# Optimization experiments

Measured on AMD Instinct MI355X. Metric: run time of the kernel, lower is better.

Reference implementation:

```python
import jax, jax.numpy as jnp
import numpy as np

N = 50000
D_IN = 128
D_OUT = 128
EPS = 1e-5


def setup_inputs() -> dict:
    key = jax.random.key(0)
    ks = jax.random.split(key, 10)
    x = jax.random.normal(ks[0], (N, D_IN), dtype=jnp.float32)
    edge_index = jax.random.randint(ks[1], (2, 800000), 0, N, dtype=jnp.int64)
    s_in = 1.0 / np.sqrt(D_IN)
    s_out = 1.0 / np.sqrt(D_OUT)
    return {
        "x": x,
        "edge_index": edge_index,
        # SAGEConv 1: lin_l (on aggregated neighbors, with bias), lin_r (root, no bias)
        "w1_l": jax.random.uniform(ks[2], (D_OUT, D_IN), jnp.float32, -s_in, s_in),
        "b1_l": jnp.zeros((D_OUT,), jnp.float32),
        "w1_r": jax.random.uniform(ks[3], (D_OUT, D_IN), jnp.float32, -s_in, s_in),
        # SAGEConv 2
        "w2_l": jax.random.uniform(ks[4], (D_OUT, D_OUT), jnp.float32, -s_out, s_out),
        "b2_l": jnp.zeros((D_OUT,), jnp.float32),
        "w2_r": jax.random.uniform(ks[5], (D_OUT, D_OUT), jnp.float32, -s_out, s_out),
        # BatchNorm affine params
        "bn_gamma": jnp.ones((D_OUT,), jnp.float32),
        "bn_beta": jnp.zeros((D_OUT,), jnp.float32),
    }


def _sage_conv(x, src, dst, w_l, b_l, w_r):
    # mean aggregation of source-node features into target nodes
    msg = x[src]                                              # [E, D]
    agg = jax.ops.segment_sum(msg, dst, num_segments=N)       # [N, D]
    cnt = jax.ops.segment_sum(jnp.ones((src.shape[0],), x.dtype), dst, num_segments=N)
    mean = agg / jnp.maximum(cnt, 1.0)[:, None]
    return mean @ w_l.T + b_l + x @ w_r.T


def _batch_norm(x, gamma, beta):
    mu = jnp.mean(x, axis=0)
    var = jnp.mean(jnp.square(x - mu), axis=0)  # biased, as in torch BN training
    return (x - mu) * jax.lax.rsqrt(var + EPS) * gamma + beta


def reference(x, edge_index, w1_l, b1_l, w1_r, w2_l, b2_l, w2_r, bn_gamma, bn_beta):
    src, dst = edge_index[0], edge_index[1]
    h = _sage_conv(x, src, dst, w1_l, b1_l, w1_r)
    h = _batch_norm(h, bn_gamma, bn_beta)
    h = jax.nn.relu(h)
    out = _sage_conv(h, src, dst, w2_l, b2_l, w2_r)
    return out
```

## Files before the change

kernel.cpp:

```cpp
#include <hip/hip_runtime.h>

#define D 128
#define EPS 1e-5f
#define FB_EPB 8

typedef unsigned int uint;
typedef __attribute__((ext_vector_type(4))) float f32x4;
typedef __attribute__((ext_vector_type(8))) short s16x8;

__device__ __forceinline__ uint pack_bf16(float a, float b)
{
    uint ua = __float_as_uint(a);
    uint ub = __float_as_uint(b);
    ua += 0x7FFFu + ((ua >> 16) & 1u);
    ub += 0x7FFFu + ((ub >> 16) & 1u);
    return (ua >> 16) | (ub & 0xFFFF0000u);
}
__device__ __forceinline__ float bf_lo(uint v) { return __uint_as_float(v << 16); }
__device__ __forceinline__ float bf_hi(uint v) { return __uint_as_float(v & 0xFFFF0000u); }

__global__ void prep_kernel(const float* __restrict__ x, uint* __restrict__ xb, int ncvt,
                            const float* __restrict__ w1l, const float* __restrict__ w1r,
                            const float* __restrict__ w2l, const float* __restrict__ w2r,
                            uint* __restrict__ wb1, uint* __restrict__ wb2)
{
    int idx = blockIdx.x * 256 + threadIdx.x;
    if (idx < ncvt) {
        float4 v = ((const float4*)x)[idx];
        uint2 o;
        o.x = pack_bf16(v.x, v.y);
        o.y = pack_bf16(v.z, v.w);
        ((uint2*)xb)[idx] = o;
    } else if (idx < ncvt + 8192) {
        int r = idx - ncvt;
        int layer = r >> 12;
        int rem = r & 4095;
        int lane = rem & 63;
        int knt = rem >> 6;
        int kstep = knt >> 3, nt = knt & 7;
        int nn = nt * 16 + (lane & 15);
        int kbase = kstep * 32 + (lane >> 4) * 8;
        const float* wl = layer ? w2l : w1l;
        const float* wr = layer ? w2r : w1r;
        uint* wb = layer ? wb2 : wb1;
        float v[8];
#pragma unroll
        for (int j = 0; j < 8; j++) {
            int k = kbase + j;
            v[j] = (k < D) ? wl[nn * D + k] : wr[nn * D + (k - D)];
        }
        uint4 o;
        o.x = pack_bf16(v[0], v[1]);
        o.y = pack_bf16(v[2], v[3]);
        o.z = pack_bf16(v[4], v[5]);
        o.w = pack_bf16(v[6], v[7]);
        ((uint4*)wb)[(kstep * 8 + nt) * 64 + lane] = o;
    } else if (idx < ncvt + 8192 + 32) {
        ((uint2*)xb)[ncvt + (idx - ncvt - 8192)] = make_uint2(0, 0);
    }
}

__global__ __launch_bounds__(512) void bcount_kernel(const int* __restrict__ dst,
                                                     int* __restrict__ bcnt,
                                                     int E, int nblk, int nbuck)
{
    __shared__ int cnt[128];
    int t = threadIdx.x;
    if (t < 128) cnt[t] = 0;
    __syncthreads();
    int e0 = blockIdx.x * (512 * FB_EPB);
#pragma unroll
    for (int k = 0; k < FB_EPB; k++) {
        int e = e0 + k * 512 + t;
        if (e < E) atomicAdd(&cnt[dst[e] >> 9], 1);
    }
    __syncthreads();
    if (t < nbuck) bcnt[t * nblk + blockIdx.x] = cnt[t];
}

__global__ __launch_bounds__(1024) void bscan_kernel(int* __restrict__ bcnt, int M)
{
    __shared__ int sums[1024];
    int t = threadIdx.x;
    int chunk = (M + 1023) / 1024;
    int b0 = t * chunk;
    int b1 = min(b0 + chunk, M);
    int v[32];
    int s = 0;
    for (int i = b0; i < b1; i++) { v[i - b0] = bcnt[i]; s += v[i - b0]; }
    sums[t] = s;
    __syncthreads();
    for (int off = 1; off < 1024; off <<= 1) {
        int u = (t >= off) ? sums[t - off] : 0;
        __syncthreads();
        sums[t] += u;
        __syncthreads();
    }
    int run = sums[t] - s;
    for (int i = b0; i < b1; i++) { bcnt[i] = run; run += v[i - b0]; }
    if (t == 1023) bcnt[M] = sums[1023];
}

__global__ __launch_bounds__(512) void bscatter_kernel(const int* __restrict__ src,
                                                       const int* __restrict__ dst,
                                                       const int* __restrict__ bcnt,
                                                       uint2* __restrict__ ebuf,
                                                       int E, int nblk, int nbuck)
{
    __shared__ int cnt[128], base[128];
    int t = threadIdx.x;
    if (t < 128) cnt[t] = 0;
    __syncthreads();
    int e0 = blockIdx.x * (512 * FB_EPB);
    int s[FB_EPB], d[FB_EPB], loc[FB_EPB];
#pragma unroll
    for (int k = 0; k < FB_EPB; k++) {
        int e = e0 + k * 512 + t;
        if (e < E) {
            s[k] = src[e];
            d[k] = dst[e];
            loc[k] = atomicAdd(&cnt[d[k] >> 9], 1);
        }
    }
    __syncthreads();
    if (t < nbuck) base[t] = bcnt[t * nblk + blockIdx.x];
    __syncthreads();
#pragma unroll
    for (int k = 0; k < FB_EPB; k++) {
        int e = e0 + k * 512 + t;
        if (e < E) {
            int b = d[k] >> 9;
            ebuf[base[b] + loc[k]] = make_uint2((uint)s[k], (uint)d[k]);
        }
    }
}

__global__ __launch_bounds__(512) void pbuild_kernel(const int* __restrict__ bcnt,
                                                     const uint2* __restrict__ ebuf,
                                                     int* __restrict__ rowptr,
                                                     int* __restrict__ col,
                                                     int n, int nblk, int nbuck, int M, int E)
{
    __shared__ int lcnt[512], lscan[512];
    int t = threadIdx.x;
    int b = blockIdx.x;
    int nb = b << 9;
    int e0 = bcnt[b * nblk];
    int e1 = (b + 1 < nbuck) ? bcnt[(b + 1) * nblk] : bcnt[M];
    lcnt[t] = 0;
    __syncthreads();
    for (int i = e0 + t; i < e1; i += 512)
        atomicAdd(&lcnt[(int)ebuf[i].y - nb], 1);
    __syncthreads();
    int s = lcnt[t];
    lscan[t] = s;
    __syncthreads();
    for (int off = 1; off < 512; off <<= 1) {
        int u = (t >= off) ? lscan[t - off] : 0;
        __syncthreads();
        lscan[t] += u;
        __syncthreads();
    }
    int start = e0 + lscan[t] - s;
    int ncnt = min(512, n - nb);
    if (t < ncnt) rowptr[nb + t] = start;
    if (b == nbuck - 1 && t == 0) rowptr[n] = E;
    lscan[t] = start;
    __syncthreads();
    for (int i = e0 + t; i < e1; i += 512) {
        uint2 ed = ebuf[i];
        int p = atomicAdd(&lscan[(int)ed.y - nb], 1);
        col[p] = (int)ed.x;
    }
}

__global__ __launch_bounds__(256) void agg_kernel(const int* __restrict__ rowptr,
                                                  const int* __restrict__ col,
                                                  const uint* __restrict__ featb,
                                                  uint* __restrict__ aggb, int n)
{
    int node = blockIdx.x * 4 + (threadIdx.x >> 6);
    if (node >= n) return;
    int lane = threadIdx.x & 63;
    int sub = lane >> 4, l16 = lane & 15;
    int r0 = rowptr[node], r1 = rowptr[node + 1];
    uint4* out4 = (uint4*)aggb;
    if (r0 == r1) {
        if (lane < 16) out4[(size_t)node * 16 + l16] = make_uint4(0, 0, 0, 0);
        return;
    }
    float acc[8] = {0.f, 0.f, 0.f, 0.f, 0.f, 0.f, 0.f, 0.f};
    const uint4* fb = (const uint4*)featb;
    int last = r1 - 1;

    for (int i = r0; i < r1; i += 16) {
        uint4 v[4];
#pragma unroll
        for (int r = 0; r < 4; r++) {
            int idx = i + r * 4 + sub;
            int cl = col[min(idx, last)];
            int c = (idx < r1) ? cl : n;
            v[r] = fb[(size_t)c * 16 + l16];
        }
#pragma unroll
        for (int r = 0; r < 4; r++) {
            uint4 u = v[r];
            acc[0] += bf_lo(u.x); acc[1] += bf_hi(u.x);
            acc[2] += bf_lo(u.y); acc[3] += bf_hi(u.y);
            acc[4] += bf_lo(u.z); acc[5] += bf_hi(u.z);
            acc[6] += bf_lo(u.w); acc[7] += bf_hi(u.w);
        }
    }
#pragma unroll
    for (int j = 0; j < 8; j++) {
        acc[j] += __shfl_down(acc[j], 32);
        acc[j] += __shfl_down(acc[j], 16);
    }
    if (lane < 16) {
        float inv = 1.0f / (float)(r1 - r0);
        uint4 o;
        o.x = pack_bf16(acc[0] * inv, acc[1] * inv);
        o.y = pack_bf16(acc[2] * inv, acc[3] * inv);
        o.z = pack_bf16(acc[4] * inv, acc[5] * inv);
        o.w = pack_bf16(acc[6] * inv, acc[7] * inv);
        out4[(size_t)node * 16 + l16] = o;
    }
}

#define TSTRIDE 132
template<bool FUSE1>
__global__ __launch_bounds__(256) void conv_kernel(
    const uint* __restrict__ p1b, const uint* __restrict__ p2b,
    const uint* __restrict__ wb, const float* __restrict__ bias,
    float* __restrict__ outf, uint* __restrict__ outb,
    float* __restrict__ pstats, int n)
{
    extern __shared__ float smem[];
    float* tile = smem;
    int w = threadIdx.x >> 6, lane = threadIdx.x & 63;
    int quad = lane >> 4, l15 = lane & 15;
    int nb = blockIdx.x * 64;

    const uint4* p1 = (const uint4*)p1b;
    const uint4* p2 = (const uint4*)p2b;
    const uint4* wv = (const uint4*)wb;

    uint4 B[8][2];
    int nt0 = w * 2;
#pragma unroll
    for (int ks = 0; ks < 8; ks++) {
#pragma unroll
        for (int t = 0; t < 2; t++)
            B[ks][t] = wv[(ks * 8 + nt0 + t) * 64 + lane];
    }

    float bv0 = bias[nt0 * 16 + l15];
    float bv1 = bias[nt0 * 16 + 16 + l15];

    for (int rt = 0; rt < 4; rt++) {
        int node = nb + rt * 16 + l15;
        int nc = min(node, n - 1);
        uint4 A[8];
#pragma unroll
        for (int ks = 0; ks < 4; ks++) A[ks] = p1[(size_t)nc * 16 + ks * 4 + quad];
#pragma unroll
        for (int ks = 0; ks < 4; ks++) A[ks + 4] = p2[(size_t)nc * 16 + ks * 4 + quad];

        f32x4 acc0 = {bv0, bv0, bv0, bv0};
        f32x4 acc1 = {bv1, bv1, bv1, bv1};
#pragma unroll
        for (int ks = 0; ks < 8; ks++) {
            s16x8 a = *(s16x8*)&A[ks];
            acc0 = __builtin_amdgcn_mfma_f32_16x16x32_bf16(a, *(s16x8*)&B[ks][0], acc0, 0, 0, 0);
            acc1 = __builtin_amdgcn_mfma_f32_16x16x32_bf16(a, *(s16x8*)&B[ks][1], acc1, 0, 0, 0);
        }
        int row0 = nb + rt * 16 + quad * 4;
        int colbase = nt0 * 16 + l15;
        if (FUSE1) {
            int rloc0 = rt * 16 + quad * 4;
#pragma unroll
            for (int reg = 0; reg < 4; reg++) {
                bool ok = (row0 + reg) < n;
                tile[(rloc0 + reg) * TSTRIDE + colbase]      = ok ? acc0[reg] : 0.f;
                tile[(rloc0 + reg) * TSTRIDE + colbase + 16] = ok ? acc1[reg] : 0.f;
            }
        } else {
#pragma unroll
            for (int reg = 0; reg < 4; reg++) {
                int row = row0 + reg;
                if (row < n) {
                    outf[(size_t)row * D + colbase] = acc0[reg];
                    outf[(size_t)row * D + colbase + 16] = acc1[reg];
                }
            }
        }
    }

    if (FUSE1) {
        __syncthreads();
        int colj = threadIdx.x & 127, half = threadIdx.x >> 7;
        float s = 0.f, ss = 0.f;
        for (int r = half * 32; r < half * 32 + 32; r++) {
            float v = tile[r * TSTRIDE + colj];
            s += v;
            ss += v * v;
        }
        float* pb = pstats + (size_t)blockIdx.x * 512 + half * 256;
        pb[colj] = s;
        pb[128 + colj] = ss;
        uint4* ob4 = (uint4*)outb;
#pragma unroll
        for (int q4 = 0; q4 < 4; q4++) {
            int idx = q4 * 256 + threadIdx.x;
            int r = idx >> 4, q = idx & 15;
            int row = nb + r;
            if (row < n) {
                float* tr = &tile[r * TSTRIDE + q * 8];
                uint4 o;
                o.x = pack_bf16(tr[0], tr[1]);
                o.y = pack_bf16(tr[2], tr[3]);
                o.z = pack_bf16(tr[4], tr[5]);
                o.w = pack_bf16(tr[6], tr[7]);
                ob4[(size_t)row * 16 + q] = o;
            }
        }
    }
}

__global__ __launch_bounds__(256) void reduce_kernel(const float* __restrict__ pstats,
                                                     float* __restrict__ stats, int nparts)
{
    int j = threadIdx.x;
    int chunk = (nparts + gridDim.x - 1) / gridDim.x;
    int p0 = blockIdx.x * chunk;
    int p1 = min(p0 + chunk, nparts);
    float s = 0.f;
    for (int p = p0; p < p1; p++) s += pstats[(size_t)p * 256 + j];
    unsafeAtomicAdd(&stats[j], s);
}

__global__ void bnfin_kernel(const float* __restrict__ stats, const float* __restrict__ gamma,
                             const float* __restrict__ beta, float* __restrict__ scsh, float n_inv)
{
    int j = threadIdx.x;
    float mean = stats[j] * n_inv;
    float var = fmaxf(stats[128 + j] * n_inv - mean * mean, 0.f);
    float sc = gamma[j] * rsqrtf(var + EPS);
    scsh[j] = sc;
    scsh[128 + j] = beta[j] - mean * sc;
}

__global__ __launch_bounds__(256) void bnapply_kernel(const uint* __restrict__ hb,
                                                      const float* __restrict__ scsh,
                                                      uint* __restrict__ hbn, int total2)
{
    __shared__ float scs[256];
    scs[threadIdx.x] = scsh[threadIdx.x];
    __syncthreads();
    int idx = blockIdx.x * 256 + threadIdx.x;
    if (blockIdx.x == 0 && threadIdx.x < 32)
        ((uint2*)hbn)[total2 + threadIdx.x] = make_uint2(0, 0);
    if (idx >= total2) return;
    int j4 = (idx & 31) * 4;
    uint2 u = ((const uint2*)hb)[idx];
    float e0 = fmaxf(bf_lo(u.x) * scs[j4 + 0] + scs[128 + j4 + 0], 0.f);
    float e1 = fmaxf(bf_hi(u.x) * scs[j4 + 1] + scs[128 + j4 + 1], 0.f);
    float e2 = fmaxf(bf_lo(u.y) * scs[j4 + 2] + scs[128 + j4 + 2], 0.f);
    float e3 = fmaxf(bf_hi(u.y) * scs[j4 + 3] + scs[128 + j4 + 3], 0.f);
    uint2 o;
    o.x = pack_bf16(e0, e1);
    o.y = pack_bf16(e2, e3);
    ((uint2*)hbn)[idx] = o;
}

extern "C" void kernel_launch(void* const* d_in, const int* in_sizes, int n_in,
                              void* d_out, int out_size, void* d_ws, size_t ws_size,
                              hipStream_t stream)
{
    const float* x     = (const float*)d_in[0];
    const int*   ei    = (const int*)d_in[1];
    const float* w1_l  = (const float*)d_in[2];
    const float* b1_l  = (const float*)d_in[3];
    const float* w1_r  = (const float*)d_in[4];
    const float* w2_l  = (const float*)d_in[5];
    const float* b2_l  = (const float*)d_in[6];
    const float* w2_r  = (const float*)d_in[7];
    const float* gamma = (const float*)d_in[8];
    const float* beta  = (const float*)d_in[9];

    int N = in_sizes[0] / D;
    int E = in_sizes[1] / 2;
    const int* src = ei;
    const int* dst = ei + E;

    int cblocks = (N + 63) / 64;
    int nbuck   = (N + 511) >> 9;
    int nblk    = (E + 4095) / 4096;
    int M       = nbuck * nblk;

    uint*  aggb   = (uint*)d_ws;
    uint*  xb     = aggb + (size_t)N * 64;
    uint*  hb     = xb + (size_t)(N + 1) * 64;
    uint*  hbn    = hb + (size_t)N * 64;
    uint*  wb1    = hbn + (size_t)(N + 1) * 64;
    uint*  wb2    = wb1 + 16384;
    uint2* ebuf   = (uint2*)(wb2 + 16384);
    float* stats  = (float*)(ebuf + E);
    float* scsh   = stats + 256;
    float* pstats = scsh + 256;
    int*   rowptr = (int*)(pstats + (size_t)cblocks * 512);
    int*   col    = rowptr + N + 1;
    int*   bcnt   = col + E;

    hipMemsetAsync(stats, 0, 256 * sizeof(float), stream);

    int ncvt = N * 32;
    int pblocks = (ncvt + 8192 + 32 + 255) / 256;
    prep_kernel<<<pblocks, 256, 0, stream>>>(x, xb, ncvt, w1_l, w1_r, w2_l, w2_r, wb1, wb2);

    int ablocks = (N + 3) / 4;

    bcount_kernel<<<nblk, 512, 0, stream>>>(dst, bcnt, E, nblk, nbuck);
    bscan_kernel<<<1, 1024, 0, stream>>>(bcnt, M);
    bscatter_kernel<<<nblk, 512, 0, stream>>>(src, dst, bcnt, ebuf, E, nblk, nbuck);
    pbuild_kernel<<<nbuck, 512, 0, stream>>>(bcnt, ebuf, rowptr, col, N, nblk, nbuck, M, E);

    agg_kernel<<<ablocks, 256, 0, stream>>>(rowptr, col, xb, aggb, N);
    conv_kernel<true><<<cblocks, 256, 64 * TSTRIDE * 4, stream>>>(
        aggb, xb, wb1, b1_l, nullptr, hb, pstats, N);

    reduce_kernel<<<32, 256, 0, stream>>>(pstats, stats, cblocks * 2);
    bnfin_kernel<<<1, 128, 0, stream>>>(stats, gamma, beta, scsh, 1.0f / (float)N);
    bnapply_kernel<<<(N * 32 + 255) / 256, 256, 0, stream>>>(hb, scsh, hbn, N * 32);

    agg_kernel<<<ablocks, 256, 0, stream>>>(rowptr, col, hbn, aggb, N);
    conv_kernel<false><<<cblocks, 256, 1024, stream>>>(
        aggb, hbn, wb2, b2_l, (float*)d_out, nullptr, nullptr, N);
}
```

Baseline: 252.0 us.

## Fold BN stat reduction into conv via last-block finalize; one node per 16 lanes in aggregation

The first conv kernel now accumulates BatchNorm sums directly into global stats with atomics. The last block to finish, found through an atomic counter, computes scale and shift itself, which removes the separate reduce and finalize launches. The aggregation kernel now maps one node to each 16-lane group instead of one per wavefront. It loads 16 neighbor indices at once, broadcasts them by shuffle, and issues 16 feature gathers per iteration, which raises memory-level parallelism and drops the cross-lane reduction. The trade-offs are float atomic contention on 256 addresses, lanes idling when node degrees in a wave differ, and higher register pressure from 16 in-flight uint4 loads.

```diff
diff --git a/kernel.cpp b/kernel.cpp
--- a/kernel.cpp
+++ b/kernel.cpp
@@ -85,9 +85,8 @@
     int chunk = (M + 1023) / 1024;
     int b0 = t * chunk;
     int b1 = min(b0 + chunk, M);
-    int v[32];
     int s = 0;
-    for (int i = b0; i < b1; i++) { v[i - b0] = bcnt[i]; s += v[i - b0]; }
+    for (int i = b0; i < b1; i++) s += bcnt[i];
     sums[t] = s;
     __syncthreads();
     for (int off = 1; off < 1024; off <<= 1) {
@@ -97,7 +96,7 @@
         __syncthreads();
     }
     int run = sums[t] - s;
-    for (int i = b0; i < b1; i++) { bcnt[i] = run; run += v[i - b0]; }
+    for (int i = b0; i < b1; i++) { int v = bcnt[i]; bcnt[i] = run; run += v; }
     if (t == 1023) bcnt[M] = sums[1023];
 }
 
@@ -174,56 +173,57 @@
     }
 }
 
-__global__ __launch_bounds__(256) void agg_kernel(const int* __restrict__ rowptr,
-                                                  const int* __restrict__ col,
-                                                  const uint* __restrict__ featb,
-                                                  uint* __restrict__ aggb, int n)
-{
-    int node = blockIdx.x * 4 + (threadIdx.x >> 6);
-    if (node >= n) return;
+__global__ __launch_bounds__(256, 4) void agg_kernel(const int* __restrict__ rowptr,
+                                                     const int* __restrict__ col,
+                                                     const uint* __restrict__ featb,
+                                                     uint* __restrict__ aggb, int n)
+{
+    int wid = threadIdx.x >> 6;
     int lane = threadIdx.x & 63;
     int sub = lane >> 4, l16 = lane & 15;
-    int r0 = rowptr[node], r1 = rowptr[node + 1];
-    uint4* out4 = (uint4*)aggb;
-    if (r0 == r1) {
-        if (lane < 16) out4[(size_t)node * 16 + l16] = make_uint4(0, 0, 0, 0);
-        return;
-    }
+    int node = blockIdx.x * 16 + wid * 4 + sub;
+    int nc = min(node, n - 1);
+    int r0 = rowptr[nc];
+    int r1 = rowptr[nc + 1];
+    int deg = (node < n) ? (r1 - r0) : 0;
+
+    int m = deg;
+    m = max(m, __shfl_xor(m, 16));
+    m = max(m, __shfl_xor(m, 32));
+    int iters = (m + 15) >> 4;
+
     float acc[8] = {0.f, 0.f, 0.f, 0.f, 0.f, 0.f, 0.f, 0.f};
     const uint4* fb = (const uint4*)featb;
-    int last = r1 - 1;
-
-    for (int i = r0; i < r1; i += 16) {
-        uint4 v[4];
-#pragma unroll
-        for (int r = 0; r < 4; r++) {
-            int idx = i + r * 4 + sub;
-            int cl = col[min(idx, last)];
-            int c = (idx < r1) ? cl : n;
-            v[r] = fb[(size_t)c * 16 + l16];
-        }
-#pragma unroll
-        for (int r = 0; r < 4; r++) {
-            uint4 u = v[r];
+    int lastc = max(r1 - 1, 0);
+
+    for (int it = 0; it < iters; ++it) {
+        int base = r0 + it * 16;
+        int cv = col[min(base + l16, lastc)];
+        uint4 v[16];
+#pragma unroll
+        for (int j = 0; j < 16; ++j) {
+            int cj = __shfl(cv, (lane & 48) | j);
+            int c = (base + j < r1) ? cj : n;
+            v[j] = fb[(size_t)c * 16 + l16];
+        }
+#pragma unroll
+        for (int j = 0; j < 16; ++j) {
+            uint4 u = v[j];
             acc[0] += bf_lo(u.x); acc[1] += bf_hi(u.x);
             acc[2] += bf_lo(u.y); acc[3] += bf_hi(u.y);
             acc[4] += bf_lo(u.z); acc[5] += bf_hi(u.z);
             acc[6] += bf_lo(u.w); acc[7] += bf_hi(u.w);
         }
     }
-#pragma unroll
-    for (int j = 0; j < 8; j++) {
-        acc[j] += __shfl_down(acc[j], 32);
-        acc[j] += __shfl_down(acc[j], 16);
-    }
-    if (lane < 16) {
-        float inv = 1.0f / (float)(r1 - r0);
+
+    if (node < n) {
+        float inv = (deg > 0) ? 1.0f / (float)deg : 0.0f;
         uint4 o;
         o.x = pack_bf16(acc[0] * inv, acc[1] * inv);
         o.y = pack_bf16(acc[2] * inv, acc[3] * inv);
         o.z = pack_bf16(acc[4] * inv, acc[5] * inv);
         o.w = pack_bf16(acc[6] * inv, acc[7] * inv);
-        out4[(size_t)node * 16 + l16] = o;
+        ((uint4*)aggb)[(size_t)node * 16 + l16] = o;
     }
 }
 
@@ -233,7 +233,9 @@
     const uint* __restrict__ p1b, const uint* __restrict__ p2b,
     const uint* __restrict__ wb, const float* __restrict__ bias,
     float* __restrict__ outf, uint* __restrict__ outb,
-    float* __restrict__ pstats, int n)
+    float* __restrict__ stats, int* __restrict__ ctr,
+    const float* __restrict__ gamma, const float* __restrict__ beta,
+    float* __restrict__ scsh, int n)
 {
     extern __shared__ float smem[];
     float* tile = smem;
@@ -259,12 +261,12 @@
 
     for (int rt = 0; rt < 4; rt++) {
         int node = nb + rt * 16 + l15;
-        int nc = min(node, n - 1);
+        int ncl = min(node, n - 1);
         uint4 A[8];
 #pragma unroll
-        for (int ks = 0; ks < 4; ks++) A[ks] = p1[(size_t)nc * 16 + ks * 4 + quad];
-#pragma unroll
-        for (int ks = 0; ks < 4; ks++) A[ks + 4] = p2[(size_t)nc * 16 + ks * 4 + quad];
+        for (int ks = 0; ks < 4; ks++) A[ks] = p1[(size_t)ncl * 16 + ks * 4 + quad];
+#pragma unroll
+        for (int ks = 0; ks < 4; ks++) A[ks + 4] = p2[(size_t)ncl * 16 + ks * 4 + quad];
 
         f32x4 acc0 = {bv0, bv0, bv0, bv0};
         f32x4 acc1 = {bv1, bv1, bv1, bv1};
@@ -297,6 +299,7 @@
     }
 
     if (FUSE1) {
+        __shared__ int lastf;
         __syncthreads();
         int colj = threadIdx.x & 127, half = threadIdx.x >> 7;
         float s = 0.f, ss = 0.f;
@@ -305,9 +308,9 @@
             s += v;
             ss += v * v;
         }
-        float* pb = pstats + (size_t)blockIdx.x * 512 + half * 256;
-        pb[colj] = s;
-        pb[128 + colj] = ss;
+        unsafeAtomicAdd(&stats[colj], s);
+        unsafeAtomicAdd(&stats[128 + colj], ss);
+
         uint4* ob4 = (uint4*)outb;
 #pragma unroll
         for (int q4 = 0; q4 < 4; q4++) {
@@ -324,30 +327,26 @@
                 ob4[(size_t)row * 16 + q] = o;
             }
         }
-    }
-}
-
-__global__ __launch_bounds__(256) void reduce_kernel(const float* __restrict__ pstats,
-                                                     float* __restrict__ stats, int nparts)
-{
-    int j = threadIdx.x;
-    int chunk = (nparts + gridDim.x - 1) / gridDim.x;
-    int p0 = blockIdx.x * chunk;
-    int p1 = min(p0 + chunk, nparts);
-    float s = 0.f;
-    for (int p = p0; p < p1; p++) s += pstats[(size_t)p * 256 + j];
-    unsafeAtomicAdd(&stats[j], s);
-}
-
-__global__ void bnfin_kernel(const float* __restrict__ stats, const float* __restrict__ gamma,
-                             const float* __restrict__ beta, float* __restrict__ scsh, float n_inv)
-{
-    int j = threadIdx.x;
-    float mean = stats[j] * n_inv;
-    float var = fmaxf(stats[128 + j] * n_inv - mean * mean, 0.f);
-    float sc = gamma[j] * rsqrtf(var + EPS);
-    scsh[j] = sc;
-    scsh[128 + j] = beta[j] - mean * sc;
+
+        __threadfence();
+        __syncthreads();
+        if (threadIdx.x == 0) {
+            int old = atomicAdd(ctr, 1);
+            lastf = (old == (int)gridDim.x - 1) ? 1 : 0;
+        }
+        __syncthreads();
+        if (lastf && threadIdx.x < 128) {
+            int j = threadIdx.x;
+            float sm = atomicAdd(&stats[j], 0.0f);
+            float sq = atomicAdd(&stats[128 + j], 0.0f);
+            float n_inv = 1.0f / (float)n;
+            float mean = sm * n_inv;
+            float var = fmaxf(sq * n_inv - mean * mean, 0.f);
+            float sc = gamma[j] * rsqrtf(var + EPS);
+            scsh[j] = sc;
+            scsh[128 + j] = beta[j] - mean * sc;
+        }
+    }
 }
 
 __global__ __launch_bounds__(256) void bnapply_kernel(const uint* __restrict__ hb,
@@ -407,18 +406,18 @@
     uint2* ebuf   = (uint2*)(wb2 + 16384);
     float* stats  = (float*)(ebuf + E);
     float* scsh   = stats + 256;
-    float* pstats = scsh + 256;
-    int*   rowptr = (int*)(pstats + (size_t)cblocks * 512);
+    int*   ctr    = (int*)(scsh + 256);
+    int*   rowptr = ctr + 1;
     int*   col    = rowptr + N + 1;
     int*   bcnt   = col + E;
 
-    hipMemsetAsync(stats, 0, 256 * sizeof(float), stream);
+    hipMemsetAsync(stats, 0, 513 * sizeof(float), stream);
 
     int ncvt = N * 32;
     int pblocks = (ncvt + 8192 + 32 + 255) / 256;
     prep_kernel<<<pblocks, 256, 0, stream>>>(x, xb, ncvt, w1_l, w1_r, w2_l, w2_r, wb1, wb2);
 
-    int ablocks = (N + 3) / 4;
+    int ablocks = (N + 15) / 16;
 
     bcount_kernel<<<nblk, 512, 0, stream>>>(dst, bcnt, E, nblk, nbuck);
     bscan_kernel<<<1, 1024, 0, stream>>>(bcnt, M);
@@ -427,13 +426,12 @@
 
     agg_kernel<<<ablocks, 256, 0, stream>>>(rowptr, col, xb, aggb, N);
     conv_kernel<true><<<cblocks, 256, 64 * TSTRIDE * 4, stream>>>(
-        aggb, xb, wb1, b1_l, nullptr, hb, pstats, N);
-
-    reduce_kernel<<<32, 256, 0, stream>>>(pstats, stats, cblocks * 2);
-    bnfin_kernel<<<1, 128, 0, stream>>>(stats, gamma, beta, scsh, 1.0f / (float)N);
+        aggb, xb, wb1, b1_l, nullptr, hb, stats, ctr, gamma, beta, scsh, N);
+
     bnapply_kernel<<<(N * 32 + 255) / 256, 256, 0, stream>>>(hb, scsh, hbn, N * 32);
 
     agg_kernel<<<ablocks, 256, 0, stream>>>(rowptr, col, hbn, aggb, N);
     conv_kernel<false><<<cblocks, 256, 1024, stream>>>(
-        aggb, hbn, wb2, b2_l, (float*)d_out, nullptr, nullptr, N);
-}
+        aggb, hbn, wb2, b2_l, (float*)d_out, nullptr, nullptr, nullptr,
+        nullptr, nullptr, nullptr, N);
+}
```

Result: slower. 356.9 us (+41.6%).
